# Performance work log

Measured on AMD Instinct MI355X. Metric: run time of the kernel, lower is better.

## Reference

```python
import jax, jax.numpy as jnp
import numpy as np

N = 100000
E = 1600000
HEADS = 4
C = 32  # per-head channels; HEADS*C = 128
NEG_SLOPE = 0.2
EPS = 1e-16


def gat_conv(x, src, dst, W, a_src, a_dst, b):
    """One PyG-style GATConv layer (concat=True, self loops already in src/dst).
    x: [N, F_in], W: [F_in, HEADS*C], a_src/a_dst: [HEADS, C], b: [HEADS*C].
    """
    h = (x @ W).reshape(N, HEADS, C)                 # [N, H, C]
    alpha_s = jnp.einsum('nhc,hc->nh', h, a_src)     # [N, H]
    alpha_d = jnp.einsum('nhc,hc->nh', h, a_dst)     # [N, H]
    e = alpha_s[src] + alpha_d[dst]                  # [E, H]
    e = jnp.where(e > 0, e, NEG_SLOPE * e)           # leaky_relu(0.2)
    # segment softmax over incoming edges of each dst node
    m = jax.ops.segment_max(e, dst, num_segments=N)  # [N, H]
    m = jnp.where(jnp.isfinite(m), m, 0.0)
    ex = jnp.exp(e - m[dst])                         # [E, H]
    denom = jax.ops.segment_sum(ex, dst, num_segments=N)
    alpha = ex / (denom[dst] + EPS)                  # [E, H]
    out = jax.ops.segment_sum(alpha[:, :, None] * h[src], dst, num_segments=N)
    return out.reshape(N, HEADS * C) + b


def setup_inputs() -> dict:
    key = jax.random.key(0)
    ks = jax.random.split(key, 6)
    x = jax.random.normal(ks[0], (N, 128), dtype=jnp.float32)
    edge_index = jax.random.randint(ks[1], (2, E), 0, N, dtype=jnp.int64)
    Ws = jax.random.normal(ks[2], (3, 128, 128), dtype=jnp.float32) * 0.1
    att_src = jax.random.normal(ks[3], (3, HEADS, C), dtype=jnp.float32) * 0.1
    att_dst = jax.random.normal(ks[4], (3, HEADS, C), dtype=jnp.float32) * 0.1
    bias = jnp.zeros((3, 128), dtype=jnp.float32)
    return {"x": x, "edge_index": edge_index, "Ws": Ws,
            "att_src": att_src, "att_dst": att_dst, "bias": bias}


def reference(x, edge_index, Ws, att_src, att_dst, bias):
    # PyG GATConv default add_self_loops=True: append i->i edges once.
    loops = jnp.arange(N, dtype=edge_index.dtype)
    src = jnp.concatenate([edge_index[0], loops])
    dst = jnp.concatenate([edge_index[1], loops])
    h = x
    n_layers = Ws.shape[0]
    for l in range(n_layers):
        h = gat_conv(h, src, dst, Ws[l], att_src[l], att_dst[l], bias[l])
        if l < n_layers - 1:
            h = jax.nn.relu(h)  # dropout p given but module run in eval -> identity
    return h
```

## Files before the change

kernel.cpp:

```cpp
#include <hip/hip_runtime.h>

#define HEADS 4
#define CPH 32
#define FDIM 128
#define NEG_SLOPE 0.2f
#define EPS_DEN 1e-16f

#define BSH 9
#define BKT (1 << BSH)
#define SCHUNK 4096


__global__ void count_kernel(const int* __restrict__ dst, int* __restrict__ deg, int E) {
    int i = blockIdx.x * blockDim.x + threadIdx.x;
    int stride = gridDim.x * blockDim.x;
    for (; i < E; i += stride) atomicAdd(&deg[dst[i]], 1);
}

__global__ void scan_sum_kernel(const int* __restrict__ deg, int* __restrict__ part, int n) {
    __shared__ int sd[256];
    int t = threadIdx.x;
    int base = blockIdx.x * 1024 + t * 4;
    int s = 0;
#pragma unroll
    for (int j = 0; j < 4; ++j) { int i = base + j; if (i < n) s += deg[i] + 1; }
    sd[t] = s;
    __syncthreads();
    for (int d = 128; d; d >>= 1) { if (t < d) sd[t] += sd[t + d]; __syncthreads(); }
    if (t == 0) part[blockIdx.x] = sd[0];
}

__global__ void scan_part_kernel(int* part, int nblk, int* row_ptr, int n) {
    if (blockIdx.x == 0 && threadIdx.x == 0) {
        int run = 0;
        for (int i = 0; i < nblk; ++i) { int v = part[i]; part[i] = run; run += v; }
        row_ptr[n] = run;
    }
}

__global__ void scan_final_kernel(const int* __restrict__ deg, const int* __restrict__ part,
                                  int* __restrict__ row_ptr, int n) {
    __shared__ int sd[256];
    int t = threadIdx.x;
    int base = blockIdx.x * 1024 + t * 4;
    int v[4]; int s = 0;
#pragma unroll
    for (int j = 0; j < 4; ++j) { int i = base + j; v[j] = (i < n) ? deg[i] + 1 : 0; s += v[j]; }
    sd[t] = s;
    __syncthreads();
    for (int d = 1; d < 256; d <<= 1) {
        int x = sd[t];
        int y = (t >= d) ? sd[t - d] : 0;
        __syncthreads();
        sd[t] = x + y;
        __syncthreads();
    }
    int off = part[blockIdx.x] + sd[t] - s;
#pragma unroll
    for (int j = 0; j < 4; ++j) {
        int i = base + j;
        if (i < n) { row_ptr[i] = off; off += v[j]; }
    }
}

__global__ void init_bcur_kernel(const int* __restrict__ row_ptr, int* __restrict__ bcur,
                                 int N, int NB) {
    int b = blockIdx.x * blockDim.x + threadIdx.x;
    if (b < NB) bcur[b] = row_ptr[min(b << BSH, N)];
}

__global__ __launch_bounds__(256) void bucket_scatter_kernel(
        const int* __restrict__ ei, int* __restrict__ bcur, int2* __restrict__ pairs,
        int E, int N, int NB) {
    __shared__ int hist[512];
    __shared__ int lcur[512];
    int ET = E + N;
    int tid = threadIdx.x;
    for (int cbase = blockIdx.x * SCHUNK; cbase < ET; cbase += gridDim.x * SCHUNK) {
        int cend = min(cbase + SCHUNK, ET);
        for (int b = tid; b < NB; b += 256) hist[b] = 0;
        __syncthreads();
        for (int i = cbase + tid; i < cend; i += 256) {
            int d = (i < E) ? ei[E + i] : (i - E);
            atomicAdd(&hist[d >> BSH], 1);
        }
        __syncthreads();
        for (int b = tid; b < NB; b += 256) {
            int c = hist[b];
            lcur[b] = c ? atomicAdd(&bcur[b], c) : 0;
        }
        __syncthreads();
        for (int i = cbase + tid; i < cend; i += 256) {
            int s, d;
            if (i < E) { s = ei[i]; d = ei[E + i]; }
            else       { s = i - E; d = s; }
            int p = atomicAdd(&lcur[d >> BSH], 1);
            pairs[p] = make_int2(s, d);
        }
        __syncthreads();
    }
}

__global__ __launch_bounds__(256) void csr_from_buckets_kernel(
        const int2* __restrict__ pairs, const int* __restrict__ row_ptr,
        int* __restrict__ csr_src, int N) {
    __shared__ int lcur[BKT];
    int lo = blockIdx.x << BSH;
    int hi = min(lo + BKT, N);
    int tid = threadIdx.x;
    for (int i = lo + tid; i < hi; i += 256) lcur[i - lo] = row_ptr[i];
    __syncthreads();
    int s0 = row_ptr[lo];
    int s1 = row_ptr[hi];
    for (int j = s0 + tid; j < s1; j += 256) {
        int2 pr = pairs[j];
        int p = atomicAdd(&lcur[pr.y - lo], 1);
        csr_src[p] = pr.x;
    }
}

#define AS_LD 68

__global__ __launch_bounds__(256) void gemm_alpha_kernel(
        const float* __restrict__ X, const float* __restrict__ W,
        const float* __restrict__ a_src, const float* __restrict__ a_dst,
        float* __restrict__ H, float* __restrict__ ASo, float* __restrict__ ADo, int n) {
    __shared__ float As[32][AS_LD];
    __shared__ float Bs[32][128];
    int tid = threadIdx.x;
    int block_row = blockIdx.x * 64;
    int cg = tid & 15;
    int rg = tid >> 4;
    int r0 = rg * 4;
    int ca = cg * 4;
    int cb = 64 + cg * 4;
    float acc[4][8];
#pragma unroll
    for (int i = 0; i < 4; ++i)
#pragma unroll
        for (int j = 0; j < 8; ++j) acc[i][j] = 0.f;

    for (int k0 = 0; k0 < 128; k0 += 32) {
        for (int t = tid; t < 512; t += 256) {
            int row = t >> 3;
            int kk = (t & 7) << 2;
            int grow = block_row + row;
            float4 v = make_float4(0.f, 0.f, 0.f, 0.f);
            if (grow < n) v = *(const float4*)&X[(size_t)grow * FDIM + k0 + kk];
            As[kk + 0][row] = v.x; As[kk + 1][row] = v.y;
            As[kk + 2][row] = v.z; As[kk + 3][row] = v.w;
        }
        for (int t = tid; t < 1024; t += 256) {
            int kr = t >> 5;
            int c4 = (t & 31) << 2;
            *(float4*)&Bs[kr][c4] = *(const float4*)&W[(size_t)(k0 + kr) * FDIM + c4];
        }
        __syncthreads();
#pragma unroll
        for (int k = 0; k < 32; ++k) {
            float4 a  = *(const float4*)&As[k][r0];
            float4 b1 = *(const float4*)&Bs[k][ca];
            float4 b2 = *(const float4*)&Bs[k][cb];
            float av[4] = {a.x, a.y, a.z, a.w};
            float bv[8] = {b1.x, b1.y, b1.z, b1.w, b2.x, b2.y, b2.z, b2.w};
#pragma unroll
            for (int i = 0; i < 4; ++i)
#pragma unroll
                for (int j = 0; j < 8; ++j) acc[i][j] = fmaf(av[i], bv[j], acc[i][j]);
        }
        __syncthreads();
    }

    int hd_a = cg >> 3;
    int hd_b = 2 + hd_a;
    int co = (cg & 7) * 4;
    float4 wsa = *(const float4*)&a_src[hd_a * CPH + co];
    float4 wsb = *(const float4*)&a_src[hd_b * CPH + co];
    float4 wda = *(const float4*)&a_dst[hd_a * CPH + co];
    float4 wdb = *(const float4*)&a_dst[hd_b * CPH + co];
#pragma unroll
    for (int i = 0; i < 4; ++i) {
        int grow = block_row + r0 + i;
        bool ok = grow < n;
        if (ok) {
            *(float4*)&H[(size_t)grow * FDIM + ca] =
                make_float4(acc[i][0], acc[i][1], acc[i][2], acc[i][3]);
            *(float4*)&H[(size_t)grow * FDIM + cb] =
                make_float4(acc[i][4], acc[i][5], acc[i][6], acc[i][7]);
        }
        float psa = acc[i][0] * wsa.x + acc[i][1] * wsa.y + acc[i][2] * wsa.z + acc[i][3] * wsa.w;
        float psb = acc[i][4] * wsb.x + acc[i][5] * wsb.y + acc[i][6] * wsb.z + acc[i][7] * wsb.w;
        float pda = acc[i][0] * wda.x + acc[i][1] * wda.y + acc[i][2] * wda.z + acc[i][3] * wda.w;
        float pdb = acc[i][4] * wdb.x + acc[i][5] * wdb.y + acc[i][6] * wdb.z + acc[i][7] * wdb.w;
#pragma unroll
        for (int off = 1; off <= 4; off <<= 1) {
            psa += __shfl_xor(psa, off);
            psb += __shfl_xor(psb, off);
            pda += __shfl_xor(pda, off);
            pdb += __shfl_xor(pdb, off);
        }
        if (ok && (cg & 7) == 0) {
            ASo[(size_t)grow * HEADS + hd_a] = psa;
            ASo[(size_t)grow * HEADS + hd_b] = psb;
            ADo[(size_t)grow * HEADS + hd_a] = pda;
            ADo[(size_t)grow * HEADS + hd_b] = pdb;
        }
    }
}

__global__ __launch_bounds__(256) void aggregate_kernel(
        const float* __restrict__ H, const float* __restrict__ ASi, const float* __restrict__ ADi,
        const int* __restrict__ row_ptr, const int* __restrict__ csr_src,
        const float* __restrict__ bias, float* __restrict__ OUT, int n, int relu) {
    int wid = (int)((blockIdx.x * (size_t)blockDim.x + threadIdx.x) >> 6);
    if (wid >= n) return;
    int lane = threadIdx.x & 63;
    int half = lane >> 5;
    int lq   = lane & 31;
    int head = lq >> 3;
    int c0   = lq << 2;

    int start = row_ptr[wid];
    int end   = row_ptr[wid + 1];
    float4 adv = *(const float4*)&ADi[(size_t)wid * HEADS];

    float m = -INFINITY;
    float dn = 0.f;
    float a0 = 0.f, a1 = 0.f, a2 = 0.f, a3 = 0.f;

    for (int base = start; base < end; base += 64) {
        int cnt = min(64, end - base);
        int idx = base + lane;
        float e0 = -INFINITY, e1 = -INFINITY, e2 = -INFINITY, e3 = -INFINITY;
        int my_src = 0;
        if (idx < end) {
            my_src = csr_src[idx];
            float4 as = *(const float4*)&ASi[(size_t)my_src * HEADS];
            float t;
            t = as.x + adv.x; e0 = t > 0.f ? t : NEG_SLOPE * t;
            t = as.y + adv.y; e1 = t > 0.f ? t : NEG_SLOPE * t;
            t = as.z + adv.z; e2 = t > 0.f ? t : NEG_SLOPE * t;
            t = as.w + adv.w; e3 = t > 0.f ? t : NEG_SLOPE * t;
        }
        float q0 = e0, q1 = e1, q2 = e2, q3 = e3;
#pragma unroll
        for (int off = 32; off; off >>= 1) {
            q0 = fmaxf(q0, __shfl_xor(q0, off));
            q1 = fmaxf(q1, __shfl_xor(q1, off));
            q2 = fmaxf(q2, __shfl_xor(q2, off));
            q3 = fmaxf(q3, __shfl_xor(q3, off));
        }
        float cm = head == 0 ? q0 : head == 1 ? q1 : head == 2 ? q2 : q3;
        float nm = fmaxf(m, cm);
        float s = __expf(m - nm);
        a0 *= s; a1 *= s; a2 *= s; a3 *= s; dn *= s;
        m = nm;
        float m0 = __shfl(m, 0), m1 = __shfl(m, 8), m2 = __shfl(m, 16), m3 = __shfl(m, 24);
        float x0 = __expf(e0 - m0);
        float x1 = __expf(e1 - m1);
        float x2 = __expf(e2 - m2);
        float x3 = __expf(e3 - m3);

        int hs = (cnt + 1) >> 1;
        float4 va = make_float4(0.f, 0.f, 0.f, 0.f);
        float4 vb = make_float4(0.f, 0.f, 0.f, 0.f);
        int sA = half;
        if (sA < cnt) {
            int sidx = __shfl(my_src, sA);
            va = *(const float4*)&H[(size_t)sidx * FDIM + c0];
        }
        int sB = half + 2;
        if (sB < cnt) {
            int sidx = __shfl(my_src, sB);
            vb = *(const float4*)&H[(size_t)sidx * FDIM + c0];
        }
        for (int j = 0; j < hs; ++j) {
            int sc = 2 * j + half;
            float t0 = __shfl(x0, sc), t1 = __shfl(x1, sc);
            float t2 = __shfl(x2, sc), t3 = __shfl(x3, sc);
            float xh = head == 0 ? t0 : head == 1 ? t1 : head == 2 ? t2 : t3;
            float4 cv = va;
            va = vb;
            int sn = sc + 4;
            if (sn < cnt) {
                int sidx = __shfl(my_src, sn);
                vb = *(const float4*)&H[(size_t)sidx * FDIM + c0];
            }
            a0 = fmaf(xh, cv.x, a0);
            a1 = fmaf(xh, cv.y, a1);
            a2 = fmaf(xh, cv.z, a2);
            a3 = fmaf(xh, cv.w, a3);
            dn += xh;
        }
    }

    a0 += __shfl_xor(a0, 32);
    a1 += __shfl_xor(a1, 32);
    a2 += __shfl_xor(a2, 32);
    a3 += __shfl_xor(a3, 32);
    dn += __shfl_xor(dn, 32);

    if (half == 0) {
        float inv = 1.f / (dn + EPS_DEN);
        float4 bv = *(const float4*)&bias[c0];
        float o0 = fmaf(a0, inv, bv.x);
        float o1 = fmaf(a1, inv, bv.y);
        float o2 = fmaf(a2, inv, bv.z);
        float o3 = fmaf(a3, inv, bv.w);
        if (relu) {
            o0 = fmaxf(o0, 0.f); o1 = fmaxf(o1, 0.f);
            o2 = fmaxf(o2, 0.f); o3 = fmaxf(o3, 0.f);
        }
        *(float4*)&OUT[(size_t)wid * FDIM + c0] = make_float4(o0, o1, o2, o3);
    }
}


extern "C" void kernel_launch(void* const* d_in, const int* in_sizes, int n_in,
                              void* d_out, int out_size, void* d_ws, size_t ws_size,
                              hipStream_t stream) {
    const int N = in_sizes[0] / FDIM;
    const int E = in_sizes[1] / 2;
    const int NB = (N + BKT - 1) >> BSH;

    const float* x    = (const float*)d_in[0];
    const int*   ei   = (const int*)d_in[1];
    const float* Ws   = (const float*)d_in[2];
    const float* asrc = (const float*)d_in[3];
    const float* adst = (const float*)d_in[4];
    const float* bias = (const float*)d_in[5];
    float* out = (float*)d_out;

    char* w = (char*)d_ws;
    auto carve = [&](size_t bytes) -> void* {
        void* p = (void*)w;
        w += (bytes + 255) & ~(size_t)255;
        return p;
    };
    float* hA      = (float*)carve((size_t)N * FDIM * 4);
    float* hB      = (float*)carve((size_t)N * FDIM * 4);
    float* ASb     = (float*)carve((size_t)N * HEADS * 4);
    float* ADb     = (float*)carve((size_t)N * HEADS * 4);
    int*   deg     = (int*)carve((size_t)N * 4);
    int*   row_ptr = (int*)carve((size_t)(N + 1) * 4);
    int*   csr_src = (int*)carve((size_t)(E + N) * 4);
    int*   part    = (int*)carve(4096);
    int*   bcur    = (int*)carve(4096);
    int2*  pairs   = (int2*)hB;

    hipMemsetAsync(deg, 0, (size_t)N * 4, stream);
    count_kernel<<<2048, 256, 0, stream>>>(ei + E, deg, E);
    int nblk = (N + 1023) / 1024;
    scan_sum_kernel<<<nblk, 256, 0, stream>>>(deg, part, N);
    scan_part_kernel<<<1, 64, 0, stream>>>(part, nblk, row_ptr, N);
    scan_final_kernel<<<nblk, 256, 0, stream>>>(deg, part, row_ptr, N);
    init_bcur_kernel<<<(NB + 255) / 256, 256, 0, stream>>>(row_ptr, bcur, N, NB);
    int sblk = min(416, (E + N + SCHUNK - 1) / SCHUNK);
    bucket_scatter_kernel<<<sblk, 256, 0, stream>>>(ei, bcur, pairs, E, N, NB);
    csr_from_buckets_kernel<<<NB, 256, 0, stream>>>(pairs, row_ptr, csr_src, N);

    const float* X = x;
    for (int l = 0; l < 3; ++l) {
        gemm_alpha_kernel<<<(N + 63) / 64, 256, 0, stream>>>(
            X, Ws + (size_t)l * FDIM * FDIM, asrc + l * HEADS * CPH, adst + l * HEADS * CPH,
            hA, ASb, ADb, N);
        float* O = (l == 2) ? out : hB;
        aggregate_kernel<<<(N + 3) / 4, 256, 0, stream>>>(
            hA, ASb, ADb, row_ptr, csr_src, bias + (size_t)l * FDIM, O, N, (l < 2) ? 1 : 0);
        X = hB;
    }
}
```

Before: 797.6 us.

## Build CSR via bucket-level counts and per-bucket local scan

```diff
diff --git a/kernel.cpp b/kernel.cpp
--- a/kernel.cpp
+++ b/kernel.cpp
@@ -11,62 +11,35 @@
 #define SCHUNK 4096
 
 
-__global__ void count_kernel(const int* __restrict__ dst, int* __restrict__ deg, int E) {
-    int i = blockIdx.x * blockDim.x + threadIdx.x;
+__global__ __launch_bounds__(256) void bucket_count_kernel(
+        const int* __restrict__ ei, int* __restrict__ bcnt, int E, int N, int NB) {
+    __shared__ int hist[512];
+    int tid = threadIdx.x;
+    int ET = E + N;
+    for (int b = tid; b < 512; b += 256) hist[b] = 0;
+    __syncthreads();
+    int i = blockIdx.x * blockDim.x + tid;
     int stride = gridDim.x * blockDim.x;
-    for (; i < E; i += stride) atomicAdd(&deg[dst[i]], 1);
-}
-
-__global__ void scan_sum_kernel(const int* __restrict__ deg, int* __restrict__ part, int n) {
-    __shared__ int sd[256];
-    int t = threadIdx.x;
-    int base = blockIdx.x * 1024 + t * 4;
-    int s = 0;
-#pragma unroll
-    for (int j = 0; j < 4; ++j) { int i = base + j; if (i < n) s += deg[i] + 1; }
-    sd[t] = s;
-    __syncthreads();
-    for (int d = 128; d; d >>= 1) { if (t < d) sd[t] += sd[t + d]; __syncthreads(); }
-    if (t == 0) part[blockIdx.x] = sd[0];
-}
-
-__global__ void scan_part_kernel(int* part, int nblk, int* row_ptr, int n) {
+    for (; i < ET; i += stride) {
+        int d = (i < E) ? ei[E + i] : (i - E);
+        atomicAdd(&hist[d >> BSH], 1);
+    }
+    __syncthreads();
+    for (int b = tid; b < NB; b += 256) {
+        int c = hist[b];
+        if (c) atomicAdd(&bcnt[b], c);
+    }
+}
+
+__global__ void bucket_scan_kernel(const int* __restrict__ bcnt, int* __restrict__ bbase,
+                                   int* __restrict__ bcur, int NB,
+                                   int* __restrict__ row_ptr, int N) {
     if (blockIdx.x == 0 && threadIdx.x == 0) {
         int run = 0;
-        for (int i = 0; i < nblk; ++i) { int v = part[i]; part[i] = run; run += v; }
-        row_ptr[n] = run;
-    }
-}
-
-__global__ void scan_final_kernel(const int* __restrict__ deg, const int* __restrict__ part,
-                                  int* __restrict__ row_ptr, int n) {
-    __shared__ int sd[256];
-    int t = threadIdx.x;
-    int base = blockIdx.x * 1024 + t * 4;
-    int v[4]; int s = 0;
-#pragma unroll
-    for (int j = 0; j < 4; ++j) { int i = base + j; v[j] = (i < n) ? deg[i] + 1 : 0; s += v[j]; }
-    sd[t] = s;
-    __syncthreads();
-    for (int d = 1; d < 256; d <<= 1) {
-        int x = sd[t];
-        int y = (t >= d) ? sd[t - d] : 0;
-        __syncthreads();
-        sd[t] = x + y;
-        __syncthreads();
-    }
-    int off = part[blockIdx.x] + sd[t] - s;
-#pragma unroll
-    for (int j = 0; j < 4; ++j) {
-        int i = base + j;
-        if (i < n) { row_ptr[i] = off; off += v[j]; }
-    }
-}
-
-__global__ void init_bcur_kernel(const int* __restrict__ row_ptr, int* __restrict__ bcur,
-                                 int N, int NB) {
-    int b = blockIdx.x * blockDim.x + threadIdx.x;
-    if (b < NB) bcur[b] = row_ptr[min(b << BSH, N)];
+        for (int b = 0; b < NB; ++b) { bbase[b] = run; bcur[b] = run; run += bcnt[b]; }
+        bbase[NB] = run;
+        row_ptr[N] = run;
+    }
 }
 
 __global__ __launch_bounds__(256) void bucket_scatter_kernel(
@@ -102,19 +75,45 @@
 }
 
 __global__ __launch_bounds__(256) void csr_from_buckets_kernel(
-        const int2* __restrict__ pairs, const int* __restrict__ row_ptr,
-        int* __restrict__ csr_src, int N) {
-    __shared__ int lcur[BKT];
-    int lo = blockIdx.x << BSH;
+        const int2* __restrict__ pairs, const int* __restrict__ bbase,
+        int* __restrict__ row_ptr, int* __restrict__ csr_src, int N) {
+    __shared__ int hist[BKT];
+    __shared__ int ssum[256];
+    int b  = blockIdx.x;
+    int lo = b << BSH;
     int hi = min(lo + BKT, N);
+    int nn = hi - lo;
     int tid = threadIdx.x;
-    for (int i = lo + tid; i < hi; i += 256) lcur[i - lo] = row_ptr[i];
-    __syncthreads();
-    int s0 = row_ptr[lo];
-    int s1 = row_ptr[hi];
+    for (int i = tid; i < BKT; i += 256) hist[i] = 0;
+    __syncthreads();
+    int s0 = bbase[b];
+    int s1 = bbase[b + 1];
+    for (int j = s0 + tid; j < s1; j += 256)
+        atomicAdd(&hist[pairs[j].y - lo], 1);
+    __syncthreads();
+    int e0 = hist[2 * tid];
+    int e1 = hist[2 * tid + 1];
+    int ps = e0 + e1;
+    ssum[tid] = ps;
+    __syncthreads();
+    for (int d = 1; d < 256; d <<= 1) {
+        int v = ssum[tid];
+        int u = (tid >= d) ? ssum[tid - d] : 0;
+        __syncthreads();
+        ssum[tid] = v + u;
+        __syncthreads();
+    }
+    int excl = ssum[tid] - ps;
+    int p0 = s0 + excl;
+    int p1 = p0 + e0;
+    if (2 * tid < nn)     row_ptr[lo + 2 * tid]     = p0;
+    if (2 * tid + 1 < nn) row_ptr[lo + 2 * tid + 1] = p1;
+    hist[2 * tid]     = p0;
+    hist[2 * tid + 1] = p1;
+    __syncthreads();
     for (int j = s0 + tid; j < s1; j += 256) {
         int2 pr = pairs[j];
-        int p = atomicAdd(&lcur[pr.y - lo], 1);
+        int p = atomicAdd(&hist[pr.y - lo], 1);
         csr_src[p] = pr.x;
     }
 }
@@ -341,23 +340,19 @@
     float* hB      = (float*)carve((size_t)N * FDIM * 4);
     float* ASb     = (float*)carve((size_t)N * HEADS * 4);
     float* ADb     = (float*)carve((size_t)N * HEADS * 4);
-    int*   deg     = (int*)carve((size_t)N * 4);
     int*   row_ptr = (int*)carve((size_t)(N + 1) * 4);
     int*   csr_src = (int*)carve((size_t)(E + N) * 4);
-    int*   part    = (int*)carve(4096);
+    int*   bcnt    = (int*)carve(4096);
+    int*   bbase   = (int*)carve(4096);
     int*   bcur    = (int*)carve(4096);
     int2*  pairs   = (int2*)hB;
 
-    hipMemsetAsync(deg, 0, (size_t)N * 4, stream);
-    count_kernel<<<2048, 256, 0, stream>>>(ei + E, deg, E);
-    int nblk = (N + 1023) / 1024;
-    scan_sum_kernel<<<nblk, 256, 0, stream>>>(deg, part, N);
-    scan_part_kernel<<<1, 64, 0, stream>>>(part, nblk, row_ptr, N);
-    scan_final_kernel<<<nblk, 256, 0, stream>>>(deg, part, row_ptr, N);
-    init_bcur_kernel<<<(NB + 255) / 256, 256, 0, stream>>>(row_ptr, bcur, N, NB);
+    hipMemsetAsync(bcnt, 0, (size_t)NB * 4, stream);
+    bucket_count_kernel<<<1024, 256, 0, stream>>>(ei, bcnt, E, N, NB);
+    bucket_scan_kernel<<<1, 64, 0, stream>>>(bcnt, bbase, bcur, NB, row_ptr, N);
     int sblk = min(416, (E + N + SCHUNK - 1) / SCHUNK);
     bucket_scatter_kernel<<<sblk, 256, 0, stream>>>(ei, bcur, pairs, E, N, NB);
-    csr_from_buckets_kernel<<<NB, 256, 0, stream>>>(pairs, row_ptr, csr_src, N);
+    csr_from_buckets_kernel<<<NB, 256, 0, stream>>>(pairs, bbase, row_ptr, csr_src, N);
 
     const float* X = x;
     for (int l = 0; l < 3; ++l) {
```

After: 749.6 us. 6.0% less time.
